# Performance work log

Hardware: AMD Instinct MI355X
Metric: run time of the kernel (lower is better)

The kernel has to match this reference:

```python
import jax, jax.numpy as jnp
import numpy as np

N_NODES = 100000
N_EDGES = 600000
DIM = 128


def setup_inputs() -> dict:
    key = jax.random.key(0)
    ks = jax.random.split(key, 7)
    scale = 1.0 / np.sqrt(DIM)
    h = jax.random.normal(ks[0], (N_NODES, DIM), dtype=jnp.float32)
    edges = jax.random.randint(ks[1], (2, N_EDGES), 0, N_NODES, dtype=jnp.int32)
    Wq = jax.random.normal(ks[2], (DIM, DIM), dtype=jnp.float32) * scale
    Wk = jax.random.normal(ks[3], (DIM, DIM), dtype=jnp.float32) * scale
    Wv = jax.random.normal(ks[4], (DIM, DIM), dtype=jnp.float32) * scale
    Wp = jax.random.normal(ks[5], (DIM, DIM), dtype=jnp.float32) * scale
    bp = jnp.zeros((DIM,), dtype=jnp.float32)
    return {"h": h, "edges": edges, "Wq": Wq, "Wk": Wk, "Wv": Wv, "Wp": Wp, "bp": bp}


def reference(h, edges, Wq, Wk, Wv, Wp, bp):
    src, dst = edges[0], edges[1]
    N, d = h.shape
    # Linear projections (nn.Linear applies x @ W.T)
    q = h @ Wq.T
    k = h @ Wk.T
    v = h @ Wv.T
    # per-edge attention logits: [E]
    scores = jnp.sum(q[dst] * k[src], axis=1) / jnp.sqrt(jnp.asarray(d, h.dtype))
    # segment softmax over incoming edges of each dst node
    max_per_dst = jax.ops.segment_max(scores, dst, num_segments=N)  # -inf for empty segments
    exp = jnp.exp(jnp.clip(scores - max_per_dst[dst], -50.0, 50.0))
    sum_per_dst = jax.ops.segment_sum(exp, dst, num_segments=N)
    alpha = exp / (sum_per_dst[dst] + 1e-9)
    alpha = jnp.nan_to_num(alpha, nan=0.0, posinf=0.0, neginf=0.0)
    # weighted message aggregation: [N, d]
    agg = jax.ops.segment_sum(v[src] * alpha[:, None], dst, num_segments=N)
    # output projection + residual + ReLU (dropout=0, bn=Identity)
    return jax.nn.relu(agg @ Wp.T + bp + h)
```

## Files before the change

kernel.cpp:

```cpp
#include <hip/hip_runtime.h>
#include <hip/hip_bf16.h>

typedef unsigned short u16;
typedef unsigned int u32;
typedef short bf16x8 __attribute__((ext_vector_type(8)));
typedef float f32x4 __attribute__((ext_vector_type(4)));

__device__ __forceinline__ float bf2f(u32 bits16) {
    return __uint_as_float(bits16 << 16);
}
__device__ __forceinline__ u16 f2bf(float f) {
    u32 u = __float_as_uint(f);
    u32 r = (u + 0x7fffu + ((u >> 16) & 1u)) >> 16;
    return (u16)r;
}

__global__ void k_conv_h(const float* __restrict__ h, u16* __restrict__ hbf, int total) {
    int i = (blockIdx.x * blockDim.x + threadIdx.x) * 4;
    if (i < total) {
        float4 val = *(const float4*)(h + i);
        u32 lo = ((u32)f2bf(val.y) << 16) | f2bf(val.x);
        u32 hi = ((u32)f2bf(val.w) << 16) | f2bf(val.z);
        uint2 o; o.x = lo; o.y = hi;
        *(uint2*)(hbf + i) = o;
    }
}

__global__ void k_prep(const float* __restrict__ Wq, const float* __restrict__ Wk,
                       const float* __restrict__ Wv, const float* __restrict__ Wp,
                       u16* __restrict__ B1, u16* __restrict__ Wpbf) {
    int j = blockIdx.x;
    int k = threadIdx.x;
    if (j < 128) {
        float s = 0.f;
        for (int t = 0; t < 128; t++) s += Wq[t * 128 + k] * Wk[t * 128 + j];
        B1[j * 128 + k] = f2bf(s);
    } else if (j < 256) {
        B1[j * 128 + k] = f2bf(Wv[(j - 128) * 128 + k]);
    } else {
        Wpbf[(j - 256) * 128 + k] = f2bf(Wp[(j - 256) * 128 + k]);
    }
}

__global__ void k_hist(const int* __restrict__ edges, int* __restrict__ deg,
                       int* __restrict__ erank, int E) {
    int e = blockIdx.x * blockDim.x + threadIdx.x;
    if (e < E) {
        int dst = edges[E + e];
        erank[e] = atomicAdd(&deg[dst], 1);
    }
}

__global__ void k_scan_part(const int* __restrict__ deg, int* __restrict__ bsum, int N) {
    __shared__ int red[256];
    int b = blockIdx.x, t = threadIdx.x;
    int i0 = b * 1024 + t * 4;
    int s = 0;
    if (i0 + 3 < N) {
        int4 v = *(const int4*)(deg + i0);
        s = v.x + v.y + v.z + v.w;
    } else {
        for (int k = 0; k < 4; k++) if (i0 + k < N) s += deg[i0 + k];
    }
    red[t] = s;
    __syncthreads();
    for (int off = 128; off > 0; off >>= 1) {
        if (t < off) red[t] += red[t + off];
        __syncthreads();
    }
    if (t == 0) bsum[b] = red[0];
}

__global__ void k_scan_top(int* __restrict__ bsum, int* __restrict__ offs, int NB, int N) {
    __shared__ int tmp[256];
    int t = threadIdx.x;
    int v = (t < NB) ? bsum[t] : 0;
    tmp[t] = v;
    __syncthreads();
    for (int off = 1; off < 256; off <<= 1) {
        int cur = tmp[t];
        int a = (t >= off) ? tmp[t - off] : 0;
        __syncthreads();
        tmp[t] = cur + a;
        __syncthreads();
    }
    if (t < NB) bsum[t] = tmp[t] - v;
    if (t == 255) offs[N] = tmp[255];
}

__global__ void k_scan_down(const int* __restrict__ deg, const int* __restrict__ bsum,
                            int* __restrict__ offs, int N) {
    __shared__ int tmp[256];
    int b = blockIdx.x, t = threadIdx.x;
    int i0 = b * 1024 + t * 4;
    int d0 = 0, d1 = 0, d2 = 0, d3 = 0;
    if (i0 + 3 < N) {
        int4 v = *(const int4*)(deg + i0);
        d0 = v.x; d1 = v.y; d2 = v.z; d3 = v.w;
    } else {
        if (i0 < N)     d0 = deg[i0];
        if (i0 + 1 < N) d1 = deg[i0 + 1];
        if (i0 + 2 < N) d2 = deg[i0 + 2];
        if (i0 + 3 < N) d3 = deg[i0 + 3];
    }
    int s = d0 + d1 + d2 + d3;
    tmp[t] = s;
    __syncthreads();
    for (int off = 1; off < 256; off <<= 1) {
        int cur = tmp[t];
        int a = (t >= off) ? tmp[t - off] : 0;
        __syncthreads();
        tmp[t] = cur + a;
        __syncthreads();
    }
    int run = bsum[b] + tmp[t] - s;
    if (i0 < N)     offs[i0]     = run; run += d0;
    if (i0 + 1 < N) offs[i0 + 1] = run; run += d1;
    if (i0 + 2 < N) offs[i0 + 2] = run; run += d2;
    if (i0 + 3 < N) offs[i0 + 3] = run;
}

__global__ void k_scatter(const int* __restrict__ edges, const int* __restrict__ offs,
                          const int* __restrict__ erank, int* __restrict__ esrc, int E) {
    int e = blockIdx.x * blockDim.x + threadIdx.x;
    if (e < E) {
        int dst = edges[E + e];
        esrc[offs[dst] + erank[e]] = edges[e];
    }
}

__launch_bounds__(256)
__global__ void k_gemm1(const u16* __restrict__ hbf, const u16* __restrict__ B1,
                        u16* __restrict__ g, u16* __restrict__ v, int N) {
    __shared__ u16 As[64 * 128];
    __shared__ u16 Bs[128 * 128];
    int tid = threadIdx.x;
    int rowBase = blockIdx.x * 64;
    int chunk = tid & 15, r0 = tid >> 4;

    for (int it = 0; it < 4; it++) {
        int r = r0 + it * 16;
        int gr = rowBase + r;
        uint4 val = make_uint4(0, 0, 0, 0);
        if (gr < N) val = *(const uint4*)(hbf + (size_t)gr * 128 + chunk * 8);
        *(uint4*)&As[r * 128 + ((chunk * 8) ^ ((r & 7) << 3))] = val;
    }

    int w = tid >> 6, l = tid & 63;
    int lr = l & 15, lq = l >> 4;

    for (int half = 0; half < 2; half++) {
        if (half) __syncthreads();
        for (int it = 0; it < 8; it++) {
            int r = r0 + it * 16;
            uint4 val = *(const uint4*)(B1 + (size_t)(half * 128 + r) * 128 + chunk * 8);
            *(uint4*)&Bs[r * 128 + ((chunk * 8) ^ ((r & 7) << 3))] = val;
        }
        __syncthreads();

        bf16x8 a[4];
        int ar = w * 16 + lr;
        for (int kk = 0; kk < 4; kk++)
            a[kk] = *(const bf16x8*)&As[ar * 128 + ((kk * 32 + lq * 8) ^ ((ar & 7) << 3))];

        for (int ct = 0; ct < 8; ct++) {
            int br = ct * 16 + lr;
            f32x4 acc = {0.f, 0.f, 0.f, 0.f};
            for (int kk = 0; kk < 4; kk++) {
                bf16x8 b = *(const bf16x8*)&Bs[br * 128 + ((kk * 32 + lq * 8) ^ ((br & 7) << 3))];
                acc = __builtin_amdgcn_mfma_f32_16x16x32_bf16(a[kk], b, acc, 0, 0, 0);
            }
            int j = ct * 16 + lr;
            for (int ri = 0; ri < 4; ri++) {
                int row = rowBase + w * 16 + lq * 4 + ri;
                if (row < N) {
                    u16 bv = f2bf(acc[ri]);
                    if (half == 0) g[(size_t)row * 128 + j] = bv;
                    else           v[(size_t)row * 128 + j] = bv;
                }
            }
        }
    }
}

__launch_bounds__(256)
__global__ void k_edge(const u16* __restrict__ g, const u16* __restrict__ hbf,
                       const u16* __restrict__ vbf, const int* __restrict__ offs,
                       const int* __restrict__ esrc, u16* __restrict__ agg, int N) {
    int wid = (blockIdx.x * blockDim.x + threadIdx.x) >> 6;
    int lane = threadIdx.x & 63;
    if (wid >= N) return;
    int sub = lane >> 4;
    int sl  = lane & 15;
    const uint4* g16 = (const uint4*)g;
    const uint4* h16 = (const uint4*)hbf;
    const uint4* v16 = (const uint4*)vbf;

    uint4 gv = g16[(size_t)wid * 16 + sl];
    float gf0 = bf2f(gv.x & 0xffff), gf1 = bf2f(gv.x >> 16);
    float gf2 = bf2f(gv.y & 0xffff), gf3 = bf2f(gv.y >> 16);
    float gf4 = bf2f(gv.z & 0xffff), gf5 = bf2f(gv.z >> 16);
    float gf6 = bf2f(gv.w & 0xffff), gf7 = bf2f(gv.w >> 16);

    int e0 = offs[wid], e1 = offs[wid + 1];
    float acc[8] = {0.f, 0.f, 0.f, 0.f, 0.f, 0.f, 0.f, 0.f};
    float denom = 0.f;
    const float sc = 0.08838834764831845f;

    for (int base = e0; base < e1; base += 4) {
        int i = base + sub;
        bool act = (i < e1);
        int src = act ? esrc[i] : 0;
        uint4 hv = h16[(size_t)src * 16 + sl];
        float p;
        p  = gf0 * bf2f(hv.x & 0xffff) + gf1 * bf2f(hv.x >> 16);
        p += gf2 * bf2f(hv.y & 0xffff) + gf3 * bf2f(hv.y >> 16);
        p += gf4 * bf2f(hv.z & 0xffff) + gf5 * bf2f(hv.z >> 16);
        p += gf6 * bf2f(hv.w & 0xffff) + gf7 * bf2f(hv.w >> 16);
        p += __shfl_xor(p, 1, 64);
        p += __shfl_xor(p, 2, 64);
        p += __shfl_xor(p, 4, 64);
        p += __shfl_xor(p, 8, 64);
        float ew = act ? __expf(p * sc) : 0.f;
        denom += ew;
        uint4 vv = v16[(size_t)src * 16 + sl];
        acc[0] += ew * bf2f(vv.x & 0xffff); acc[1] += ew * bf2f(vv.x >> 16);
        acc[2] += ew * bf2f(vv.y & 0xffff); acc[3] += ew * bf2f(vv.y >> 16);
        acc[4] += ew * bf2f(vv.z & 0xffff); acc[5] += ew * bf2f(vv.z >> 16);
        acc[6] += ew * bf2f(vv.w & 0xffff); acc[7] += ew * bf2f(vv.w >> 16);
    }

    for (int m = 16; m < 64; m <<= 1) {
        denom += __shfl_xor(denom, m, 64);
        for (int k = 0; k < 8; k++) acc[k] += __shfl_xor(acc[k], m, 64);
    }

    if (sub == 0) {
        float inv = (denom > 0.f) ? 1.f / denom : 0.f;
        uint4 o;
        o.x = ((u32)f2bf(acc[1] * inv) << 16) | f2bf(acc[0] * inv);
        o.y = ((u32)f2bf(acc[3] * inv) << 16) | f2bf(acc[2] * inv);
        o.z = ((u32)f2bf(acc[5] * inv) << 16) | f2bf(acc[4] * inv);
        o.w = ((u32)f2bf(acc[7] * inv) << 16) | f2bf(acc[6] * inv);
        ((uint4*)agg)[(size_t)wid * 16 + sl] = o;
    }
}

__launch_bounds__(256)
__global__ void k_gemm2(const u16* __restrict__ aggbf, const u16* __restrict__ Wpbf,
                        const float* __restrict__ bp, const float* __restrict__ h,
                        float* __restrict__ out, int N) {
    __shared__ u16 As[64 * 128];
    __shared__ u16 Bs[128 * 128];
    int tid = threadIdx.x;
    int rowBase = blockIdx.x * 64;
    int chunk = tid & 15, r0 = tid >> 4;

    for (int it = 0; it < 4; it++) {
        int r = r0 + it * 16;
        int gr = rowBase + r;
        uint4 val = make_uint4(0, 0, 0, 0);
        if (gr < N) val = *(const uint4*)(aggbf + (size_t)gr * 128 + chunk * 8);
        *(uint4*)&As[r * 128 + ((chunk * 8) ^ ((r & 7) << 3))] = val;
    }
    for (int it = 0; it < 8; it++) {
        int r = r0 + it * 16;
        uint4 val = *(const uint4*)(Wpbf + (size_t)r * 128 + chunk * 8);
        *(uint4*)&Bs[r * 128 + ((chunk * 8) ^ ((r & 7) << 3))] = val;
    }
    __syncthreads();

    int w = tid >> 6, l = tid & 63;
    int lr = l & 15, lq = l >> 4;
    bf16x8 a[4];
    int ar = w * 16 + lr;
    for (int kk = 0; kk < 4; kk++)
        a[kk] = *(const bf16x8*)&As[ar * 128 + ((kk * 32 + lq * 8) ^ ((ar & 7) << 3))];

    for (int ct = 0; ct < 8; ct++) {
        int br = ct * 16 + lr;
        f32x4 acc = {0.f, 0.f, 0.f, 0.f};
        for (int kk = 0; kk < 4; kk++) {
            bf16x8 b = *(const bf16x8*)&Bs[br * 128 + ((kk * 32 + lq * 8) ^ ((br & 7) << 3))];
            acc = __builtin_amdgcn_mfma_f32_16x16x32_bf16(a[kk], b, acc, 0, 0, 0);
        }
        int j = ct * 16 + lr;
        float bj = bp[j];
        for (int ri = 0; ri < 4; ri++) {
            int row = rowBase + w * 16 + lq * 4 + ri;
            if (row < N) {
                float val = acc[ri] + bj + h[(size_t)row * 128 + j];
                out[(size_t)row * 128 + j] = fmaxf(val, 0.f);
            }
        }
    }
}

extern "C" void kernel_launch(void* const* d_in, const int* in_sizes, int n_in,
                              void* d_out, int out_size, void* d_ws, size_t ws_size,
                              hipStream_t stream) {
    const float* h  = (const float*)d_in[0];
    const int* edges = (const int*)d_in[1];
    const float* Wq = (const float*)d_in[2];
    const float* Wk = (const float*)d_in[3];
    const float* Wv = (const float*)d_in[4];
    const float* Wp = (const float*)d_in[5];
    const float* bp = (const float*)d_in[6];
    float* out = (float*)d_out;

    int N = in_sizes[0] / 128;
    int E = in_sizes[1] / 2;

    char* ws = (char*)d_ws;
    size_t off = 0;
    auto alloc = [&](size_t bytes) -> char* {
        char* p = ws + off;
        off = (off + bytes + 255) & ~(size_t)255;
        return p;
    };
    u16* hbf  = (u16*)alloc((size_t)N * 128 * 2);
    u16* B1   = (u16*)alloc(256 * 128 * 2);
    u16* Wpbf = (u16*)alloc(128 * 128 * 2);
    u16* g    = (u16*)alloc((size_t)N * 128 * 2);
    u16* v    = (u16*)alloc((size_t)N * 128 * 2);
    u16* agg  = (u16*)alloc((size_t)N * 128 * 2);
    int* deg   = (int*)alloc((size_t)N * 4);
    int* offs  = (int*)alloc((size_t)(N + 1) * 4);
    int* erank = (int*)alloc((size_t)E * 4);
    int* esrc  = (int*)alloc((size_t)E * 4);
    int* bsum  = (int*)alloc(256 * 4);
    (void)ws_size; (void)n_in; (void)out_size;

    hipMemsetAsync(deg, 0, (size_t)N * 4, stream);

    int NB = (N + 1023) / 1024;
    int total = N * 128;
    k_conv_h<<<(total / 4 + 255) / 256, 256, 0, stream>>>(h, hbf, total);
    k_prep<<<384, 128, 0, stream>>>(Wq, Wk, Wv, Wp, B1, Wpbf);
    k_hist<<<(E + 255) / 256, 256, 0, stream>>>(edges, deg, erank, E);
    k_scan_part<<<NB, 256, 0, stream>>>(deg, bsum, N);
    k_scan_top<<<1, 256, 0, stream>>>(bsum, offs, NB, N);
    k_scan_down<<<NB, 256, 0, stream>>>(deg, bsum, offs, N);
    k_scatter<<<(E + 255) / 256, 256, 0, stream>>>(edges, offs, erank, esrc, E);
    k_gemm1<<<(N + 63) / 64, 256, 0, stream>>>(hbf, B1, g, v, N);
    k_edge<<<(N + 3) / 4, 256, 0, stream>>>(g, hbf, v, offs, esrc, agg, N);
    k_gemm2<<<(N + 63) / 64, 256, 0, stream>>>(agg, Wpbf, bp, h, out, N);
}
```

Before: 278.3 us.

## Fold Wv into output projection and aggregate h directly in edge kernel

Precomputes Wp·Wv as a single bf16 weight so the edge kernel aggregates attention-weighted source features h instead of projected values v. This removes the v projection from the first GEMM, the v buffer write, and the second random gather per edge. The residual in the final GEMM also reads the bf16 copy of h instead of fp32. The trade-off is that the fused weight is rounded to bf16 and the residual uses lower precision, which changes numerics slightly.

```diff
diff --git a/kernel.cpp b/kernel.cpp
--- a/kernel.cpp
+++ b/kernel.cpp
@@ -28,17 +28,18 @@
 
 __global__ void k_prep(const float* __restrict__ Wq, const float* __restrict__ Wk,
                        const float* __restrict__ Wv, const float* __restrict__ Wp,
-                       u16* __restrict__ B1, u16* __restrict__ Wpbf) {
+                       u16* __restrict__ B1, u16* __restrict__ Wpv) {
     int j = blockIdx.x;
     int k = threadIdx.x;
     if (j < 128) {
         float s = 0.f;
         for (int t = 0; t < 128; t++) s += Wq[t * 128 + k] * Wk[t * 128 + j];
         B1[j * 128 + k] = f2bf(s);
-    } else if (j < 256) {
-        B1[j * 128 + k] = f2bf(Wv[(j - 128) * 128 + k]);
     } else {
-        Wpbf[(j - 256) * 128 + k] = f2bf(Wp[(j - 256) * 128 + k]);
+        int m = j - 128;
+        float s = 0.f;
+        for (int t = 0; t < 128; t++) s += Wp[m * 128 + t] * Wv[t * 128 + k];
+        Wpv[m * 128 + k] = f2bf(s);
     }
 }
 
@@ -131,7 +132,7 @@
 
 __launch_bounds__(256)
 __global__ void k_gemm1(const u16* __restrict__ hbf, const u16* __restrict__ B1,
-                        u16* __restrict__ g, u16* __restrict__ v, int N) {
+                        u16* __restrict__ g, int N) {
     __shared__ u16 As[64 * 128];
     __shared__ u16 Bs[128 * 128];
     int tid = threadIdx.x;
@@ -145,48 +146,39 @@
         if (gr < N) val = *(const uint4*)(hbf + (size_t)gr * 128 + chunk * 8);
         *(uint4*)&As[r * 128 + ((chunk * 8) ^ ((r & 7) << 3))] = val;
     }
+    for (int it = 0; it < 8; it++) {
+        int r = r0 + it * 16;
+        uint4 val = *(const uint4*)(B1 + (size_t)r * 128 + chunk * 8);
+        *(uint4*)&Bs[r * 128 + ((chunk * 8) ^ ((r & 7) << 3))] = val;
+    }
+    __syncthreads();
 
     int w = tid >> 6, l = tid & 63;
     int lr = l & 15, lq = l >> 4;
-
-    for (int half = 0; half < 2; half++) {
-        if (half) __syncthreads();
-        for (int it = 0; it < 8; it++) {
-            int r = r0 + it * 16;
-            uint4 val = *(const uint4*)(B1 + (size_t)(half * 128 + r) * 128 + chunk * 8);
-            *(uint4*)&Bs[r * 128 + ((chunk * 8) ^ ((r & 7) << 3))] = val;
+    bf16x8 a[4];
+    int ar = w * 16 + lr;
+    for (int kk = 0; kk < 4; kk++)
+        a[kk] = *(const bf16x8*)&As[ar * 128 + ((kk * 32 + lq * 8) ^ ((ar & 7) << 3))];
+
+    for (int ct = 0; ct < 8; ct++) {
+        int br = ct * 16 + lr;
+        f32x4 acc = {0.f, 0.f, 0.f, 0.f};
+        for (int kk = 0; kk < 4; kk++) {
+            bf16x8 b = *(const bf16x8*)&Bs[br * 128 + ((kk * 32 + lq * 8) ^ ((br & 7) << 3))];
+            acc = __builtin_amdgcn_mfma_f32_16x16x32_bf16(a[kk], b, acc, 0, 0, 0);
         }
-        __syncthreads();
-
-        bf16x8 a[4];
-        int ar = w * 16 + lr;
-        for (int kk = 0; kk < 4; kk++)
-            a[kk] = *(const bf16x8*)&As[ar * 128 + ((kk * 32 + lq * 8) ^ ((ar & 7) << 3))];
-
-        for (int ct = 0; ct < 8; ct++) {
-            int br = ct * 16 + lr;
-            f32x4 acc = {0.f, 0.f, 0.f, 0.f};
-            for (int kk = 0; kk < 4; kk++) {
-                bf16x8 b = *(const bf16x8*)&Bs[br * 128 + ((kk * 32 + lq * 8) ^ ((br & 7) << 3))];
-                acc = __builtin_amdgcn_mfma_f32_16x16x32_bf16(a[kk], b, acc, 0, 0, 0);
-            }
-            int j = ct * 16 + lr;
-            for (int ri = 0; ri < 4; ri++) {
-                int row = rowBase + w * 16 + lq * 4 + ri;
-                if (row < N) {
-                    u16 bv = f2bf(acc[ri]);
-                    if (half == 0) g[(size_t)row * 128 + j] = bv;
-                    else           v[(size_t)row * 128 + j] = bv;
-                }
-            }
+        int j = ct * 16 + lr;
+        for (int ri = 0; ri < 4; ri++) {
+            int row = rowBase + w * 16 + lq * 4 + ri;
+            if (row < N) g[(size_t)row * 128 + j] = f2bf(acc[ri]);
         }
     }
 }
 
 __launch_bounds__(256)
 __global__ void k_edge(const u16* __restrict__ g, const u16* __restrict__ hbf,
-                       const u16* __restrict__ vbf, const int* __restrict__ offs,
-                       const int* __restrict__ esrc, u16* __restrict__ agg, int N) {
+                       const int* __restrict__ offs, const int* __restrict__ esrc,
+                       u16* __restrict__ agg, int N) {
     int wid = (blockIdx.x * blockDim.x + threadIdx.x) >> 6;
     int lane = threadIdx.x & 63;
     if (wid >= N) return;
@@ -194,7 +186,6 @@
     int sl  = lane & 15;
     const uint4* g16 = (const uint4*)g;
     const uint4* h16 = (const uint4*)hbf;
-    const uint4* v16 = (const uint4*)vbf;
 
     uint4 gv = g16[(size_t)wid * 16 + sl];
     float gf0 = bf2f(gv.x & 0xffff), gf1 = bf2f(gv.x >> 16);
@@ -212,22 +203,22 @@
         bool act = (i < e1);
         int src = act ? esrc[i] : 0;
         uint4 hv = h16[(size_t)src * 16 + sl];
-        float p;
-        p  = gf0 * bf2f(hv.x & 0xffff) + gf1 * bf2f(hv.x >> 16);
-        p += gf2 * bf2f(hv.y & 0xffff) + gf3 * bf2f(hv.y >> 16);
-        p += gf4 * bf2f(hv.z & 0xffff) + gf5 * bf2f(hv.z >> 16);
-        p += gf6 * bf2f(hv.w & 0xffff) + gf7 * bf2f(hv.w >> 16);
+        float h0 = bf2f(hv.x & 0xffff), h1 = bf2f(hv.x >> 16);
+        float h2 = bf2f(hv.y & 0xffff), h3 = bf2f(hv.y >> 16);
+        float h4 = bf2f(hv.z & 0xffff), h5 = bf2f(hv.z >> 16);
+        float h6 = bf2f(hv.w & 0xffff), h7 = bf2f(hv.w >> 16);
+        float p = gf0 * h0 + gf1 * h1 + gf2 * h2 + gf3 * h3
+                + gf4 * h4 + gf5 * h5 + gf6 * h6 + gf7 * h7;
         p += __shfl_xor(p, 1, 64);
         p += __shfl_xor(p, 2, 64);
         p += __shfl_xor(p, 4, 64);
         p += __shfl_xor(p, 8, 64);
         float ew = act ? __expf(p * sc) : 0.f;
         denom += ew;
-        uint4 vv = v16[(size_t)src * 16 + sl];
-        acc[0] += ew * bf2f(vv.x & 0xffff); acc[1] += ew * bf2f(vv.x >> 16);
-        acc[2] += ew * bf2f(vv.y & 0xffff); acc[3] += ew * bf2f(vv.y >> 16);
-        acc[4] += ew * bf2f(vv.z & 0xffff); acc[5] += ew * bf2f(vv.z >> 16);
-        acc[6] += ew * bf2f(vv.w & 0xffff); acc[7] += ew * bf2f(vv.w >> 16);
+        acc[0] += ew * h0; acc[1] += ew * h1;
+        acc[2] += ew * h2; acc[3] += ew * h3;
+        acc[4] += ew * h4; acc[5] += ew * h5;
+        acc[6] += ew * h6; acc[7] += ew * h7;
     }
 
     for (int m = 16; m < 64; m <<= 1) {
@@ -247,8 +238,8 @@
 }
 
 __launch_bounds__(256)
-__global__ void k_gemm2(const u16* __restrict__ aggbf, const u16* __restrict__ Wpbf,
-                        const float* __restrict__ bp, const float* __restrict__ h,
+__global__ void k_gemm2(const u16* __restrict__ aggbf, const u16* __restrict__ Wpv,
+                        const float* __restrict__ bp, const u16* __restrict__ hbf,
                         float* __restrict__ out, int N) {
     __shared__ u16 As[64 * 128];
     __shared__ u16 Bs[128 * 128];
@@ -265,7 +256,7 @@
     }
     for (int it = 0; it < 8; it++) {
         int r = r0 + it * 16;
-        uint4 val = *(const uint4*)(Wpbf + (size_t)r * 128 + chunk * 8);
+        uint4 val = *(const uint4*)(Wpv + (size_t)r * 128 + chunk * 8);
         *(uint4*)&Bs[r * 128 + ((chunk * 8) ^ ((r & 7) << 3))] = val;
     }
     __syncthreads();
@@ -289,7 +280,8 @@
         for (int ri = 0; ri < 4; ri++) {
             int row = rowBase + w * 16 + lq * 4 + ri;
             if (row < N) {
-                float val = acc[ri] + bj + h[(size_t)row * 128 + j];
+                float res = bf2f(hbf[(size_t)row * 128 + j]);
+                float val = acc[ri] + bj + res;
                 out[(size_t)row * 128 + j] = fmaxf(val, 0.f);
             }
         }
@@ -319,10 +311,9 @@
         return p;
     };
     u16* hbf  = (u16*)alloc((size_t)N * 128 * 2);
-    u16* B1   = (u16*)alloc(256 * 128 * 2);
-    u16* Wpbf = (u16*)alloc(128 * 128 * 2);
+    u16* B1   = (u16*)alloc(128 * 128 * 2);
+    u16* Wpv  = (u16*)alloc(128 * 128 * 2);
     u16* g    = (u16*)alloc((size_t)N * 128 * 2);
-    u16* v    = (u16*)alloc((size_t)N * 128 * 2);
     u16* agg  = (u16*)alloc((size_t)N * 128 * 2);
     int* deg   = (int*)alloc((size_t)N * 4);
     int* offs  = (int*)alloc((size_t)(N + 1) * 4);
@@ -336,13 +327,13 @@
     int NB = (N + 1023) / 1024;
     int total = N * 128;
     k_conv_h<<<(total / 4 + 255) / 256, 256, 0, stream>>>(h, hbf, total);
-    k_prep<<<384, 128, 0, stream>>>(Wq, Wk, Wv, Wp, B1, Wpbf);
+    k_prep<<<256, 128, 0, stream>>>(Wq, Wk, Wv, Wp, B1, Wpv);
     k_hist<<<(E + 255) / 256, 256, 0, stream>>>(edges, deg, erank, E);
     k_scan_part<<<NB, 256, 0, stream>>>(deg, bsum, N);
     k_scan_top<<<1, 256, 0, stream>>>(bsum, offs, NB, N);
     k_scan_down<<<NB, 256, 0, stream>>>(deg, bsum, offs, N);
     k_scatter<<<(E + 255) / 256, 256, 0, stream>>>(edges, offs, erank, esrc, E);
-    k_gemm1<<<(N + 63) / 64, 256, 0, stream>>>(hbf, B1, g, v, N);
-    k_edge<<<(N + 3) / 4, 256, 0, stream>>>(g, hbf, v, offs, esrc, agg, N);
-    k_gemm2<<<(N + 63) / 64, 256, 0, stream>>>(agg, Wpbf, bp, h, out, N);
-}
+    k_gemm1<<<(N + 63) / 64, 256, 0, stream>>>(hbf, B1, g, N);
+    k_edge<<<(N + 3) / 4, 256, 0, stream>>>(g, hbf, offs, esrc, agg, N);
+    k_gemm2<<<(N + 63) / 64, 256, 0, stream>>>(agg, Wpv, bp, hbf, out, N);
+}
```

New measurement: 253.8 us. 1.1x faster.
